# Kernel tuning notes

Measured on AMD Instinct MI355X. Metric: run time of the kernel, lower is better.

## Reference

```python
import jax, jax.numpy as jnp
import numpy as np

B = 8192      # batch of matchups
L = 40        # history_len
HN = 32       # hist_numeric_dim
TE = 96       # team_embed_dim
SE = 32       # seed_embed_dim
HH = 64       # hist_hidden_dim
NH = 4        # num_heads
HD = HH // NH # head dim = 16
MID = 128     # middle_dim
BOX = 8       # box_score_dim
NT = 400      # num_teams
NS = 17       # num_seeds
TOWER_IN = TE + SE + 1 + 2 * HH  # 257
MERGED = 2 * MID                 # 256
EPS = 1e-5


def setup_inputs() -> dict:
    key = jax.random.key(0)
    ks = iter(jax.random.split(key, 80))
    nrm = lambda shape, s=0.05: (jax.random.normal(next(ks), shape, jnp.float32) * s)
    inp = {}
    inp['teamA_id'] = jax.random.randint(next(ks), (B,), 1, NT)
    inp['teamB_id'] = jax.random.randint(next(ks), (B,), 1, NT)
    inp['teamA_seed'] = jax.random.randint(next(ks), (B,), 0, NS)
    inp['teamB_seed'] = jax.random.randint(next(ks), (B,), 0, NS)
    inp['teamA_elo'] = 1500.0 + 200.0 * jax.random.normal(next(ks), (B,), jnp.float32)
    inp['teamB_elo'] = 1500.0 + 200.0 * jax.random.normal(next(ks), (B,), jnp.float32)
    inp['teamA_hist_numeric'] = jax.random.normal(next(ks), (B, L, HN), jnp.float32)
    inp['teamB_hist_numeric'] = jax.random.normal(next(ks), (B, L, HN), jnp.float32)
    inp['teamA_hist_opp_ids'] = jax.random.randint(next(ks), (B, L), 0, NT)
    inp['teamB_hist_opp_ids'] = jax.random.randint(next(ks), (B, L), 0, NT)
    # 0/1 padding mask; guarantee at least one valid game per row
    inp['teamA_hist_mask'] = (jax.random.uniform(next(ks), (B, L)) < 0.8).astype(jnp.float32).at[:, 0].set(1.0)
    inp['teamB_hist_mask'] = (jax.random.uniform(next(ks), (B, L)) < 0.8).astype(jnp.float32).at[:, 0].set(1.0)
    # parameters
    inp['team_emb'] = nrm((NT, TE), 0.1).at[0].set(0.0)  # padding_idx=0
    inp['seed_emb'] = nrm((NS, SE), 0.1)
    inp['conv_w'] = nrm((HH, HN + TE, 3))
    inp['conv_b'] = nrm((HH,))
    inp['cbn_g'] = jnp.ones((HH,)); inp['cbn_b'] = jnp.zeros((HH,))
    inp['cbn_rm'] = nrm((HH,), 0.01); inp['cbn_rv'] = jnp.ones((HH,))
    inp['hp_w'] = nrm((HH, HN + TE)); inp['hp_b'] = nrm((HH,))
    inp['qp_w'] = nrm((HH, TE)); inp['qp_b'] = nrm((HH,))
    inp['attn_in_w'] = nrm((3 * HH, HH)); inp['attn_in_b'] = nrm((3 * HH,))
    inp['attn_out_w'] = nrm((HH, HH)); inp['attn_out_b'] = nrm((HH,))
    inp['ln_g'] = jnp.ones((HH,)); inp['ln_b'] = jnp.zeros((HH,))
    inp['tw_w'] = nrm((MID, TOWER_IN)); inp['tw_b'] = nrm((MID,))
    inp['tbn_g'] = jnp.ones((MID,)); inp['tbn_b'] = jnp.zeros((MID,))
    inp['tbn_rm'] = nrm((MID,), 0.01); inp['tbn_rv'] = jnp.ones((MID,))
    inp['r1_w'] = nrm((MERGED, MERGED)); inp['r1_b'] = nrm((MERGED,))
    inp['r1bn_g'] = jnp.ones((MERGED,)); inp['r1bn_b'] = jnp.zeros((MERGED,))
    inp['r1bn_rm'] = nrm((MERGED,), 0.01); inp['r1bn_rv'] = jnp.ones((MERGED,))
    inp['r2_w'] = nrm((MERGED, MERGED)); inp['r2_b'] = nrm((MERGED,))
    inp['r2bn_g'] = jnp.ones((MERGED,)); inp['r2bn_b'] = jnp.zeros((MERGED,))
    inp['r2bn_rm'] = nrm((MERGED,), 0.01); inp['r2bn_rv'] = jnp.ones((MERGED,))
    inp['mu_w'] = nrm((BOX, MERGED)); inp['mu_b'] = nrm((BOX,))
    inp['lv_w'] = nrm((BOX, MERGED)); inp['lv_b'] = nrm((BOX,))
    inp['wl_w'] = nrm((1, MERGED)); inp['wl_b'] = nrm((1,))
    return inp


def _bn(x, g, b, rm, rv):
    # eval-mode BatchNorm over last axis
    return (x - rm) * jax.lax.rsqrt(rv + EPS) * g + b


def _ln(x, g, b):
    m = jnp.mean(x, axis=-1, keepdims=True)
    v = jnp.var(x, axis=-1, keepdims=True)
    return (x - m) * jax.lax.rsqrt(v + EPS) * g + b


def reference(teamA_id, teamB_id, teamA_seed, teamB_seed, teamA_elo, teamB_elo,
              teamA_hist_numeric, teamA_hist_opp_ids, teamA_hist_mask,
              teamB_hist_numeric, teamB_hist_opp_ids, teamB_hist_mask,
              team_emb, seed_emb, conv_w, conv_b, cbn_g, cbn_b, cbn_rm, cbn_rv,
              hp_w, hp_b, qp_w, qp_b, attn_in_w, attn_in_b, attn_out_w, attn_out_b,
              ln_g, ln_b, tw_w, tw_b, tbn_g, tbn_b, tbn_rm, tbn_rv,
              r1_w, r1_b, r1bn_g, r1bn_b, r1bn_rm, r1bn_rv,
              r2_w, r2_b, r2bn_g, r2bn_b, r2bn_rm, r2bn_rv,
              mu_w, mu_b, lv_w, lv_b, wl_w, wl_b):
    silu = jax.nn.silu

    def attend(q_emb, hn, opp, mask):
        m = mask[..., None]
        x = jnp.concatenate([hn * m, team_emb[opp] * m], axis=-1)      # [B,L,HN+TE]
        res = silu(x @ hp_w.T + hp_b)                                   # [B,L,HH]
        c = jax.lax.conv_general_dilated(
            x.transpose(0, 2, 1), conv_w, (1,), [(1, 1)],
            dimension_numbers=('NCH', 'OIH', 'NCH')) + conv_b[:, None]  # [B,HH,L]
        c = _bn(c.transpose(0, 2, 1), cbn_g, cbn_b, cbn_rm, cbn_rv)     # [B,L,HH]
        kv = silu(c + res)                                              # [B,L,HH]
        q = q_emb @ qp_w.T + qp_b                                       # [B,HH]
        wq, wk, wv = jnp.split(attn_in_w, 3, axis=0)
        bq, bk, bv = jnp.split(attn_in_b, 3, axis=0)
        qh = (q @ wq.T + bq).reshape(-1, NH, HD)
        kh = (kv @ wk.T + bk).reshape(-1, L, NH, HD)
        vh = (kv @ wv.T + bv).reshape(-1, L, NH, HD)
        scores = jnp.einsum('bhd,blhd->bhl', qh, kh) / np.float32(np.sqrt(HD))
        scores = jnp.where(mask[:, None, :] > 0.0, scores, -1e9)
        a = jax.nn.softmax(scores, axis=-1)
        o = jnp.einsum('bhl,blhd->bhd', a, vh).reshape(-1, HH)
        o = o @ attn_out_w.T + attn_out_b
        return _ln(o + q, ln_g, ln_b)

    ea = team_emb[teamA_id]
    eb = team_emb[teamB_id]
    sa = seed_emb[teamA_seed]
    sb = seed_emb[teamB_seed]
    za = (teamA_elo[:, None] - 1500.0) / 400.0
    zb = (teamB_elo[:, None] - 1500.0) / 400.0

    aa = attend(ea, teamA_hist_numeric, teamA_hist_opp_ids, teamA_hist_mask)
    ab = attend(ea, teamB_hist_numeric, teamB_hist_opp_ids, teamB_hist_mask)
    bb = attend(eb, teamB_hist_numeric, teamB_hist_opp_ids, teamB_hist_mask)
    ba = attend(eb, teamA_hist_numeric, teamA_hist_opp_ids, teamA_hist_mask)

    ta = jnp.concatenate([ea, sa, za, aa, ab], axis=-1)
    tb = jnp.concatenate([eb, sb, zb, bb, ba], axis=-1)

    tower = lambda t: silu(_bn(t @ tw_w.T + tw_b, tbn_g, tbn_b, tbn_rm, tbn_rv))
    ra = tower(ta)
    rb = tower(tb)

    x = jnp.concatenate([ra - rb, ra * rb], axis=-1)
    x = silu(_bn(x @ r1_w.T + r1_b, r1bn_g, r1bn_b, r1bn_rm, r1bn_rv)) + x
    x = silu(_bn(x @ r2_w.T + r2_b, r2bn_g, r2bn_b, r2bn_rm, r2bn_rv)) + x

    box_mu = x @ mu_w.T + mu_b
    box_log_var = x @ lv_w.T + lv_b
    win_logit = (x @ wl_w.T + wl_b)[:, 0]
    return ((box_mu, box_log_var), win_logit)
```

## Files before the change

### kernel.cpp

```cpp
#include <hip/hip_runtime.h>
#include <stdint.h>

#define EPS 1e-5f

typedef __attribute__((ext_vector_type(8))) short short8;
typedef __attribute__((ext_vector_type(4))) float floatx4;
typedef __attribute__((ext_vector_type(4))) unsigned uintx4;
typedef unsigned short u16;

__device__ __forceinline__ u16 f2bf(float f) {
  unsigned u = __builtin_bit_cast(unsigned, f);
  u += 0x7fffu + ((u >> 16) & 1u);
  return (u16)(u >> 16);
}
__device__ __forceinline__ float bf2f(u16 h) {
  return __builtin_bit_cast(float, (unsigned)h << 16);
}
__device__ __forceinline__ unsigned pack2bf(float a, float b) {
  return (unsigned)f2bf(a) | ((unsigned)f2bf(b) << 16);
}
__device__ __forceinline__ float silu_f(float x) { return x / (1.f + __expf(-x)); }
__device__ __forceinline__ float wave_sum(float x) {
  for (int off = 32; off > 0; off >>= 1) x += __shfl_xor(x, off);
  return x;
}

__global__ void prep_kernel(const float* __restrict__ hp_w, const float* __restrict__ conv_w,
                            const float* __restrict__ attn_in_w,
                            const float* __restrict__ attn_out_w,
                            const float* __restrict__ tw_w, const float* __restrict__ r1_w,
                            const float* __restrict__ r2_w,
                            u16* __restrict__ w1f, u16* __restrict__ w2f,
                            float* __restrict__ woT,
                            float* __restrict__ twT, float* __restrict__ r1T,
                            float* __restrict__ r2T) {
  int t = blockIdx.x * 256 + threadIdx.x;
  if (t < 32768) {
    int j = t & 7, lane = (t >> 3) & 63, ks = (t >> 9) & 3, nt = (t >> 11) & 3, tp = t >> 13;
    int k = ks * 32 + ((lane >> 4) << 3) + j;
    int c = nt * 16 + (lane & 15);
    float v = (tp == 3) ? hp_w[c * 128 + k] : conv_w[c * 384 + k * 3 + tp];
    w1f[t] = f2bf(v);
  }
  if (t < 8192) {
    int j = t & 7, lane = (t >> 3) & 63, ks = (t >> 9) & 1, nt = t >> 10;
    int k = ks * 32 + ((lane >> 4) << 3) + j;
    int n = nt * 16 + (lane & 15);
    w2f[t] = f2bf(attn_in_w[(64 + n) * 64 + k]);
  }
  if (t < 1024) {
    int j = t & 63, k4 = t >> 6;
#pragma unroll
    for (int i = 0; i < 4; ++i)
      woT[(k4 * 64 + j) * 4 + i] = attn_out_w[j * 64 + k4 * 4 + i];
  }
  if (t < 8320) {
    int mid = t & 127, k4 = t >> 7;
#pragma unroll
    for (int i = 0; i < 4; ++i) {
      int k = k4 * 4 + i;
      twT[t * 4 + i] = (k < 257) ? tw_w[mid * 257 + k] : 0.f;
    }
  }
  if (t < 16384) {
    int o = t & 255, k4 = t >> 8;
#pragma unroll
    for (int i = 0; i < 4; ++i) {
      r1T[t * 4 + i] = r1_w[o * 256 + k4 * 4 + i];
      r2T[t * 4 + i] = r2_w[o * 256 + k4 * 4 + i];
    }
  }
}

__global__ __launch_bounds__(64) void team_kernel(
    const float* __restrict__ temb, const float* __restrict__ qp_w,
    const float* __restrict__ qp_b, const float* __restrict__ attn_in_w,
    const float* __restrict__ attn_in_b,
    float* __restrict__ Qg, float* __restrict__ QHg) {
  __shared__ float e[96];
  __shared__ float qv[64];
  const int t = blockIdx.x;
  const int o = threadIdx.x;
  for (int i = o; i < 96; i += 64) e[i] = temb[t * 96 + i];
  __syncthreads();
  float acc = qp_b[o];
  for (int k = 0; k < 96; ++k) acc += e[k] * qp_w[o * 96 + k];
  qv[o] = acc;
  Qg[t * 64 + o] = acc;
  __syncthreads();
  float acc2 = attn_in_b[o];
  for (int k = 0; k < 64; ++k) acc2 += qv[k] * attn_in_w[o * 64 + k];
  QHg[t * 64 + o] = acc2;
}

__global__ __launch_bounds__(256, 2) void attn_kernel(
    const int* __restrict__ idA, const int* __restrict__ idB,
    const float* __restrict__ hnA, const float* __restrict__ hnB,
    const int* __restrict__ oppA, const int* __restrict__ oppB,
    const float* __restrict__ mskA, const float* __restrict__ mskB,
    const float* __restrict__ temb, const float* __restrict__ conv_b,
    const float* __restrict__ cbn_g, const float* __restrict__ cbn_b,
    const float* __restrict__ cbn_rm, const float* __restrict__ cbn_rv,
    const float* __restrict__ hp_b,
    const float* __restrict__ attn_in_b, const float* __restrict__ attn_out_b,
    const float* __restrict__ ln_g, const float* __restrict__ ln_b,
    const u16* __restrict__ w1f, const u16* __restrict__ w2f,
    const float* __restrict__ woT,
    const float* __restrict__ Qg, const float* __restrict__ QHg,
    float* __restrict__ ATT) {
  __shared__ __align__(16) u16 arena[19488];
  __shared__ __align__(16) float qh_s[2 * 64];
  u16* xs = arena;
  u16* kvb = arena + 5712;
  float* KVP = (float*)(arena + 9168);
  float* a_s = (float*)(arena + 5712);
  float* op = a_s + 8 * 40;

  const int tid = threadIdx.x;
  const int lane = tid & 63;
  const int wv = tid >> 6;
  const int qd = lane >> 4;
  const int l16 = lane & 15;
  const int qw = wv >> 1;
  const int hw = wv & 1;

  const int c_lane = wv * 16 + l16;
  const float sc_c = rsqrtf(cbn_rv[c_lane] + EPS) * cbn_g[c_lane];
  const float sh_c = cbn_b[c_lane] - cbn_rm[c_lane] * sc_c;
  const float hpb_c = hp_b[c_lane];
  const float cvb_c = conv_b[c_lane];
  const float lng = ln_g[lane], lnb = ln_b[lane];
  const float aob = attn_out_b[lane];
  const float kb0 = attn_in_b[64 + (wv * 2 + 0) * 16 + l16];
  const float kb1 = attn_in_b[64 + (wv * 2 + 1) * 16 + l16];

  if (tid < 136) {
    xs[tid] = 0;
    xs[41 * 136 + tid] = 0;
  }
  __syncthreads();

  short8 w1r[4][4];
#pragma unroll
  for (int tp = 0; tp < 4; ++tp)
#pragma unroll
    for (int ks = 0; ks < 4; ++ks)
      w1r[tp][ks] = *reinterpret_cast<const short8*>(
          w1f + (((tp * 4 + wv) * 4 + ks) * 64 + lane) * 8);
  short8 w2r[2][2];
#pragma unroll
  for (int ntl = 0; ntl < 2; ++ntl)
#pragma unroll
    for (int ks = 0; ks < 2; ++ks)
      w2r[ntl][ks] = *reinterpret_cast<const short8*>(
          w2f + (((wv * 2 + ntl) * 2 + ks) * 64 + lane) * 8);

  unsigned xr[12];
  float mkr[3];
  {
    int np = blockIdx.x;
    int pb = np >> 1;
    const float* phn = (np & 1) ? hnB : hnA;
    const int* popp = (np & 1) ? oppB : oppA;
    const float* pmsk = (np & 1) ? mskB : mskA;
#pragma unroll
    for (int j = 0; j < 3; ++j) {
      int sidx = j * 256 + tid;
      int srow = sidx >> 4, scg = sidx & 15;
      if (srow < 40) {
        int mrow = pb * 40 + srow;
        mkr[j] = pmsk[mrow];
        const float* p = (scg < 4)
                             ? phn + (size_t)mrow * 32 + scg * 8
                             : temb + (size_t)popp[mrow] * 96 + (scg * 8 - 32);
        floatx4 f0 = *reinterpret_cast<const floatx4*>(p);
        floatx4 f1 = *reinterpret_cast<const floatx4*>(p + 4);
        xr[j * 4 + 0] = pack2bf(f0[0], f0[1]);
        xr[j * 4 + 1] = pack2bf(f0[2], f0[3]);
        xr[j * 4 + 2] = pack2bf(f1[0], f1[1]);
        xr[j * 4 + 3] = pack2bf(f1[2], f1[3]);
      } else {
        mkr[j] = 0.f;
        xr[j * 4 + 0] = xr[j * 4 + 1] = xr[j * 4 + 2] = xr[j * 4 + 3] = 0u;
      }
    }
  }

  float qreg = 0.f, qhreg = 0.f, m_l = 0.f;
  {
    int b0i = blockIdx.x >> 1, s0 = blockIdx.x & 1;
    if (lane < 40) m_l = (s0 ? mskB : mskA)[b0i * 40 + lane];
    if (wv < 2) {
      int id0 = wv ? idB[b0i] : idA[b0i];
      qreg = Qg[id0 * 64 + lane];
      qhreg = QHg[id0 * 64 + lane];
    }
  }

#pragma unroll 1
  for (int it = 0; it < 8; ++it) {
    int pair = blockIdx.x + it * 2048;
    int b = pair >> 1, s = pair & 1;

#pragma unroll
    for (int j = 0; j < 3; ++j) {
      int sidx = j * 256 + tid;
      int srow = sidx >> 4;
      if (srow < 40) {
        bool keep = mkr[j] != 0.f;
        uintx4 v;
        v[0] = keep ? xr[j * 4 + 0] : 0u;
        v[1] = keep ? xr[j * 4 + 1] : 0u;
        v[2] = keep ? xr[j * 4 + 2] : 0u;
        v[3] = keep ? xr[j * 4 + 3] : 0u;
        *reinterpret_cast<uintx4*>(xs + (srow + 1) * 136 + (sidx & 15) * 8) = v;
      }
    }
    __syncthreads();

    float pf[3][8];
    float mknew[3];
    {
      int np = (it < 7) ? pair + 2048 : pair;
      int pb = np >> 1;
      const float* phn = (np & 1) ? hnB : hnA;
      const int* popp = (np & 1) ? oppB : oppA;
      const float* pmsk = (np & 1) ? mskB : mskA;
#pragma unroll
      for (int j = 0; j < 3; ++j) {
        int sidx = j * 256 + tid;
        int srow = sidx >> 4, scg = sidx & 15;
        if (srow < 40) {
          int mrow = pb * 40 + srow;
          mknew[j] = pmsk[mrow];
          const float* p = (scg < 4)
                               ? phn + (size_t)mrow * 32 + scg * 8
                               : temb + (size_t)popp[mrow] * 96 + (scg * 8 - 32);
          *reinterpret_cast<floatx4*>(&pf[j][0]) = *reinterpret_cast<const floatx4*>(p);
          *reinterpret_cast<floatx4*>(&pf[j][4]) = *reinterpret_cast<const floatx4*>(p + 4);
        } else {
          mknew[j] = 0.f;
#pragma unroll
          for (int q = 0; q < 8; ++q) pf[j][q] = 0.f;
        }
      }
    }

#pragma unroll 1
    for (int mt = 0; mt < 3; ++mt) {
      floatx4 ach = {0.f, 0.f, 0.f, 0.f};
      floatx4 acv = {0.f, 0.f, 0.f, 0.f};
#pragma unroll
      for (int ks = 0; ks < 4; ++ks) {
        const u16* base = xs + (mt * 16 + l16) * 136 + ks * 32 + (qd << 3);
        short8 af0 = *reinterpret_cast<const short8*>(base);
        short8 af1 = *reinterpret_cast<const short8*>(base + 136);
        short8 af2 = *reinterpret_cast<const short8*>(base + 272);
        acv = __builtin_amdgcn_mfma_f32_16x16x32_bf16(af0, w1r[0][ks], acv, 0, 0, 0);
        acv = __builtin_amdgcn_mfma_f32_16x16x32_bf16(af1, w1r[1][ks], acv, 0, 0, 0);
        acv = __builtin_amdgcn_mfma_f32_16x16x32_bf16(af2, w1r[2][ks], acv, 0, 0, 0);
        ach = __builtin_amdgcn_mfma_f32_16x16x32_bf16(af1, w1r[3][ks], ach, 0, 0, 0);
      }
#pragma unroll
      for (int r = 0; r < 4; ++r) {
        float kv = silu_f(silu_f(ach[r] + hpb_c) + (acv[r] + cvb_c) * sc_c + sh_c);
        kvb[(mt * 16 + qd * 4 + r) * 72 + c_lane] = f2bf(kv);
      }
    }
    if (wv < 2) qh_s[wv * 64 + lane] = qhreg;
    __syncthreads();

    {
      floatx4 acc[3][2] = {};
#pragma unroll
      for (int mt = 0; mt < 3; ++mt) {
        short8 af[2];
#pragma unroll
        for (int ks = 0; ks < 2; ++ks)
          af[ks] = *reinterpret_cast<const short8*>(
              kvb + (mt * 16 + l16) * 72 + ks * 32 + (qd << 3));
#pragma unroll
        for (int ntl = 0; ntl < 2; ++ntl)
#pragma unroll
          for (int ks = 0; ks < 2; ++ks)
            acc[mt][ntl] = __builtin_amdgcn_mfma_f32_16x16x32_bf16(
                af[ks], w2r[ntl][ks], acc[mt][ntl], 0, 0, 0);
      }
#pragma unroll
      for (int mt = 0; mt < 3; ++mt)
#pragma unroll
        for (int ntl = 0; ntl < 2; ++ntl)
#pragma unroll
          for (int r = 0; r < 4; ++r) {
            int row = mt * 16 + qd * 4 + r;
            if (row < 40)
              KVP[row * 129 + (wv * 2 + ntl) * 16 + l16] =
                  acc[mt][ntl][r] + (ntl ? kb1 : kb0);
          }
    }
    __syncthreads();

#pragma unroll
    for (int j = 0; j < 3; ++j) {
      xr[j * 4 + 0] = pack2bf(pf[j][0], pf[j][1]);
      xr[j * 4 + 1] = pack2bf(pf[j][2], pf[j][3]);
      xr[j * 4 + 2] = pack2bf(pf[j][4], pf[j][5]);
      xr[j * 4 + 3] = pack2bf(pf[j][6], pf[j][7]);
      mkr[j] = mknew[j];
    }

    {
      float a2[2];
#pragma unroll
      for (int hh = 0; hh < 2; ++hh) {
        int h = hw * 2 + hh;
        float e = 0.f;
        if (lane < 40 && m_l > 0.f) {
          float s0 = 0.f, s1 = 0.f;
#pragma unroll
          for (int d = 0; d < 16; d += 2) {
            s0 += qh_s[qw * 64 + h * 16 + d] * KVP[lane * 129 + h * 16 + d];
            s1 += qh_s[qw * 64 + h * 16 + d + 1] * KVP[lane * 129 + h * 16 + d + 1];
          }
          e = __expf((s0 + s1) * 0.25f);
        }
        float sm = wave_sum(e);
        a2[hh] = e / sm;
      }
      if (lane < 40) {
        a_s[(qw * 4 + hw * 2 + 0) * 40 + lane] = a2[0];
        a_s[(qw * 4 + hw * 2 + 1) * 40 + lane] = a2[1];
      }
    }

    {
      int d = hw * 32 + (lane & 31);
      int arow = qw * 4 + (d >> 4);
      int l0 = (lane >> 5) * 20;
      float v0 = 0.f, v1 = 0.f;
#pragma unroll
      for (int li = 0; li < 20; li += 2) {
        int l = l0 + li;
        v0 += a_s[arow * 40 + l] * KVP[l * 129 + 64 + d];
        v1 += a_s[arow * 40 + l + 1] * KVP[(l + 1) * 129 + 64 + d];
      }
      float v = v0 + v1;
      v += __shfl_xor(v, 32);
      if (lane < 32) op[qw * 64 + d] = v;
    }
    __syncthreads();

    if (wv < 2) {
      int qi = wv;
      float acc0 = aob + qreg, acc1 = 0.f;
      const floatx4* wo4 = reinterpret_cast<const floatx4*>(woT);
#pragma unroll 8
      for (int k4 = 0; k4 < 16; ++k4) {
        floatx4 w4 = wo4[k4 * 64 + lane];
        floatx4 x4 = *reinterpret_cast<const floatx4*>(&op[qi * 64 + k4 * 4]);
        acc0 += x4[0] * w4[0] + x4[2] * w4[2];
        acc1 += x4[1] * w4[1] + x4[3] * w4[3];
      }
      float r = acc0 + acc1;
      float mean = wave_sum(r) * (1.f / 64.f);
      float dv = r - mean;
      float var = wave_sum(dv * dv) * (1.f / 64.f);
      float outv = dv * rsqrtf(var + EPS) * lng + lnb;
      ATT[((qi * 2 + s) * 8192 + b) * 64 + lane] = outv;
    }

    if (it < 7) {
      int bn = b + 1024;
      if (lane < 40) m_l = (s ? mskB : mskA)[bn * 40 + lane];
      if (wv < 2) {
        int idn = wv ? idB[bn] : idA[bn];
        qreg = Qg[idn * 64 + lane];
        qhreg = QHg[idn * 64 + lane];
      }
    }
  }
}

__global__ __launch_bounds__(256) void head_kernel(
    const int* __restrict__ idA, const int* __restrict__ idB,
    const int* __restrict__ seedA, const int* __restrict__ seedB,
    const float* __restrict__ eloA, const float* __restrict__ eloB,
    const float* __restrict__ temb, const float* __restrict__ semb,
    const float* __restrict__ twT, const float* __restrict__ tw_b,
    const float* __restrict__ tbn_g, const float* __restrict__ tbn_b,
    const float* __restrict__ tbn_rm, const float* __restrict__ tbn_rv,
    const float* __restrict__ r1T, const float* __restrict__ r1_b,
    const float* __restrict__ r1bn_g, const float* __restrict__ r1bn_b,
    const float* __restrict__ r1bn_rm, const float* __restrict__ r1bn_rv,
    const float* __restrict__ r2T, const float* __restrict__ r2_b,
    const float* __restrict__ r2bn_g, const float* __restrict__ r2bn_b,
    const float* __restrict__ r2bn_rm, const float* __restrict__ r2bn_rv,
    const float* __restrict__ mu_w, const float* __restrict__ mu_b,
    const float* __restrict__ lv_w, const float* __restrict__ lv_b,
    const float* __restrict__ wl_w, const float* __restrict__ wl_b,
    const float* __restrict__ ATT, float* __restrict__ out) {
  __shared__ __align__(16) float smem[12416];
  float* tv = smem;
  float* rr = smem + 8320;
  float* xv = smem;
  float* xw = smem + 4096;
  const int tid = threadIdx.x;
  const int b0 = blockIdx.x * 16;

  for (int idx = tid; idx < 2 * 16 * 260; idx += 256) {
    int k = idx % 260;
    int bi = (idx / 260) & 15;
    int team = idx / (260 * 16);
    int b = b0 + bi;
    float v;
    if (k < 96) v = temb[(team ? idB[b] : idA[b]) * 96 + k];
    else if (k < 128) v = semb[(team ? seedB[b] : seedA[b]) * 32 + (k - 96)];
    else if (k == 128) v = ((team ? eloB[b] : eloA[b]) - 1500.f) * (1.f / 400.f);
    else if (k < 193) v = ATT[((team * 2 + team) * 8192 + b) * 64 + (k - 129)];
    else if (k < 257) v = ATT[((team * 2 + (1 - team)) * 8192 + b) * 64 + (k - 193)];
    else v = 0.f;
    tv[(team * 16 + bi) * 260 + k] = v;
  }
  __syncthreads();

  {
    int team = tid >> 7, mid = tid & 127;
    const floatx4* twv = reinterpret_cast<const floatx4*>(twT);
    float acc[16];
    float b_ = tw_b[mid];
#pragma unroll
    for (int bi = 0; bi < 16; ++bi) acc[bi] = b_;
#pragma unroll 2
    for (int k4 = 0; k4 < 65; ++k4) {
      floatx4 w4 = twv[k4 * 128 + mid];
#pragma unroll
      for (int bi = 0; bi < 16; ++bi) {
        floatx4 x4 = *reinterpret_cast<const floatx4*>(&tv[(team * 16 + bi) * 260 + k4 * 4]);
        acc[bi] += x4[0] * w4[0] + x4[1] * w4[1] + x4[2] * w4[2] + x4[3] * w4[3];
      }
    }
    float sc = rsqrtf(tbn_rv[mid] + EPS) * tbn_g[mid];
    float sh = tbn_b[mid] - tbn_rm[mid] * sc;
#pragma unroll
    for (int bi = 0; bi < 16; ++bi)
      rr[(team * 16 + bi) * 128 + mid] = silu_f(acc[bi] * sc + sh);
  }
  __syncthreads();
  {
    int o = tid;
#pragma unroll
    for (int bi = 0; bi < 16; ++bi)
      xv[bi * 256 + o] = (o < 128)
                             ? (rr[bi * 128 + o] - rr[(16 + bi) * 128 + o])
                             : (rr[bi * 128 + o - 128] * rr[(16 + bi) * 128 + o - 128]);
  }
  __syncthreads();
  {
    int o = tid;
    const floatx4* r1v = reinterpret_cast<const floatx4*>(r1T);
    float acc[16];
    float b_ = r1_b[o];
#pragma unroll
    for (int bi = 0; bi < 16; ++bi) acc[bi] = b_;
#pragma unroll 2
    for (int k4 = 0; k4 < 64; ++k4) {
      floatx4 w4 = r1v[k4 * 256 + o];
#pragma unroll
      for (int bi = 0; bi < 16; ++bi) {
        floatx4 x4 = *reinterpret_cast<const floatx4*>(&xv[bi * 256 + k4 * 4]);
        acc[bi] += x4[0] * w4[0] + x4[1] * w4[1] + x4[2] * w4[2] + x4[3] * w4[3];
      }
    }
    float sc = rsqrtf(r1bn_rv[o] + EPS) * r1bn_g[o];
    float sh = r1bn_b[o] - r1bn_rm[o] * sc;
#pragma unroll
    for (int bi = 0; bi < 16; ++bi)
      xw[bi * 256 + o] = silu_f(acc[bi] * sc + sh) + xv[bi * 256 + o];
  }
  __syncthreads();
  {
    int o = tid;
    const floatx4* r2v = reinterpret_cast<const floatx4*>(r2T);
    float acc[16];
    float b_ = r2_b[o];
#pragma unroll
    for (int bi = 0; bi < 16; ++bi) acc[bi] = b_;
#pragma unroll 2
    for (int k4 = 0; k4 < 64; ++k4) {
      floatx4 w4 = r2v[k4 * 256 + o];
#pragma unroll
      for (int bi = 0; bi < 16; ++bi) {
        floatx4 x4 = *reinterpret_cast<const floatx4*>(&xw[bi * 256 + k4 * 4]);
        acc[bi] += x4[0] * w4[0] + x4[1] * w4[1] + x4[2] * w4[2] + x4[3] * w4[3];
      }
    }
    float sc = rsqrtf(r2bn_rv[o] + EPS) * r2bn_g[o];
    float sh = r2bn_b[o] - r2bn_rm[o] * sc;
#pragma unroll
    for (int bi = 0; bi < 16; ++bi)
      xv[bi * 256 + o] = silu_f(acc[bi] * sc + sh) + xw[bi * 256 + o];
  }
  __syncthreads();
  {
    int bi = tid >> 4, j = tid & 15;
    const float* wrow = (j < 8) ? (mu_w + j * 256) : (lv_w + (j - 8) * 256);
    const floatx4* wrow4 = reinterpret_cast<const floatx4*>(wrow);
    float acc = (j < 8) ? mu_b[j] : lv_b[j - 8];
#pragma unroll 4
    for (int k4 = 0; k4 < 64; ++k4) {
      floatx4 x4 = *reinterpret_cast<const floatx4*>(&xv[bi * 256 + k4 * 4]);
      floatx4 w4 = wrow4[k4];
      acc += x4[0] * w4[0] + x4[1] * w4[1] + x4[2] * w4[2] + x4[3] * w4[3];
    }
    int b = b0 + bi;
    if (j < 8) out[b * 8 + j] = acc;
    else out[65536 + b * 8 + (j - 8)] = acc;
    if (tid < 16) {
      const floatx4* wl4 = reinterpret_cast<const floatx4*>(wl_w);
      float acc2 = wl_b[0];
#pragma unroll 4
      for (int k4 = 0; k4 < 64; ++k4) {
        floatx4 x4 = *reinterpret_cast<const floatx4*>(&xv[tid * 256 + k4 * 4]);
        floatx4 w4 = wl4[k4];
        acc2 += x4[0] * w4[0] + x4[1] * w4[1] + x4[2] * w4[2] + x4[3] * w4[3];
      }
      out[131072 + b0 + tid] = acc2;
    }
  }
}

extern "C" void kernel_launch(void* const* d_in, const int* in_sizes, int n_in,
                              void* d_out, int out_size, void* d_ws, size_t ws_size,
                              hipStream_t stream) {
  const int* idA = (const int*)d_in[0];
  const int* idB = (const int*)d_in[1];
  const int* seedA = (const int*)d_in[2];
  const int* seedB = (const int*)d_in[3];
  const float* eloA = (const float*)d_in[4];
  const float* eloB = (const float*)d_in[5];
  const float* hnA = (const float*)d_in[6];
  const float* hnB = (const float*)d_in[7];
  const int* oppA = (const int*)d_in[8];
  const int* oppB = (const int*)d_in[9];
  const float* mskA = (const float*)d_in[10];
  const float* mskB = (const float*)d_in[11];
  const float* temb = (const float*)d_in[12];
  const float* semb = (const float*)d_in[13];
  const float* conv_w = (const float*)d_in[14];
  const float* conv_b = (const float*)d_in[15];
  const float* cbn_g = (const float*)d_in[16];
  const float* cbn_b = (const float*)d_in[17];
  const float* cbn_rm = (const float*)d_in[18];
  const float* cbn_rv = (const float*)d_in[19];
  const float* hp_w = (const float*)d_in[20];
  const float* hp_b = (const float*)d_in[21];
  const float* qp_w = (const float*)d_in[22];
  const float* qp_b = (const float*)d_in[23];
  const float* attn_in_w = (const float*)d_in[24];
  const float* attn_in_b = (const float*)d_in[25];
  const float* attn_out_w = (const float*)d_in[26];
  const float* attn_out_b = (const float*)d_in[27];
  const float* ln_g = (const float*)d_in[28];
  const float* ln_b = (const float*)d_in[29];
  const float* tw_w = (const float*)d_in[30];
  const float* tw_b = (const float*)d_in[31];
  const float* tbn_g = (const float*)d_in[32];
  const float* tbn_b = (const float*)d_in[33];
  const float* tbn_rm = (const float*)d_in[34];
  const float* tbn_rv = (const float*)d_in[35];
  const float* r1_w = (const float*)d_in[36];
  const float* r1_b = (const float*)d_in[37];
  const float* r1bn_g = (const float*)d_in[38];
  const float* r1bn_b = (const float*)d_in[39];
  const float* r1bn_rm = (const float*)d_in[40];
  const float* r1bn_rv = (const float*)d_in[41];
  const float* r2_w = (const float*)d_in[42];
  const float* r2_b = (const float*)d_in[43];
  const float* r2bn_g = (const float*)d_in[44];
  const float* r2bn_b = (const float*)d_in[45];
  const float* r2bn_rm = (const float*)d_in[46];
  const float* r2bn_rv = (const float*)d_in[47];
  const float* mu_w = (const float*)d_in[48];
  const float* mu_b = (const float*)d_in[49];
  const float* lv_w = (const float*)d_in[50];
  const float* lv_b = (const float*)d_in[51];
  const float* wl_w = (const float*)d_in[52];
  const float* wl_b = (const float*)d_in[53];

  char* ws = (char*)d_ws;
  u16* w1f = (u16*)(ws + 0);
  u16* w2f = (u16*)(ws + 65536);
  float* woT = (float*)(ws + 81920);
  float* Qg = (float*)(ws + 98304);
  float* QHg = (float*)(ws + 200704);
  float* twT = (float*)(ws + 303104);
  float* r1T = (float*)(ws + 436224);
  float* r2T = (float*)(ws + 698368);
  float* ATT = (float*)(ws + 960512);

  prep_kernel<<<256, 256, 0, stream>>>(hp_w, conv_w, attn_in_w, attn_out_w,
                                       tw_w, r1_w, r2_w,
                                       w1f, w2f, woT, twT, r1T, r2T);
  team_kernel<<<400, 64, 0, stream>>>(temb, qp_w, qp_b, attn_in_w, attn_in_b, Qg, QHg);
  attn_kernel<<<2048, 256, 0, stream>>>(idA, idB, hnA, hnB, oppA, oppB, mskA, mskB,
                                        temb, conv_b, cbn_g, cbn_b, cbn_rm, cbn_rv,
                                        hp_b, attn_in_b, attn_out_b, ln_g, ln_b,
                                        w1f, w2f, woT, Qg, QHg, ATT);
  head_kernel<<<512, 256, 0, stream>>>(idA, idB, seedA, seedB, eloA, eloB, temb, semb,
                                       twT, tw_b, tbn_g, tbn_b, tbn_rm, tbn_rv,
                                       r1T, r1_b, r1bn_g, r1bn_b, r1bn_rm, r1bn_rv,
                                       r2T, r2_b, r2bn_g, r2bn_b, r2bn_rm, r2bn_rv,
                                       mu_w, mu_b, lv_w, lv_b, wl_w, wl_b,
                                       ATT, (float*)d_out);
}
```

Measured before the change: 535.7 us.

## Prefetch opponent ids and query vectors one extra iteration ahead in attend loop

The opponent-id indices used for the embedding gather are now loaded two iterations ahead, so the next iteration's team-embedding loads no longer wait on a dependent index load. The per-pair query, head-query and mask loads move from the loop tail into the prefetch block, overlapping them with the MFMA work. The bf16 packing of prefetched rows moves earlier, and the initial barrier is merged with the first prefetch. This adds register pressure from extra live values.

```diff
diff --git a/kernel.cpp b/kernel.cpp
--- a/kernel.cpp
+++ b/kernel.cpp
@@ -138,7 +138,6 @@
     xs[tid] = 0;
     xs[41 * 136 + tid] = 0;
   }
-  __syncthreads();
 
   short8 w1r[4][4];
 #pragma unroll
@@ -187,6 +186,8 @@
   }
 
   float qreg = 0.f, qhreg = 0.f, m_l = 0.f;
+  int idn = 0;
+  int oppn[3];
   {
     int b0i = blockIdx.x >> 1, s0 = blockIdx.x & 1;
     if (lane < 40) m_l = (s0 ? mskB : mskA)[b0i * 40 + lane];
@@ -194,8 +195,18 @@
       int id0 = wv ? idB[b0i] : idA[b0i];
       qreg = Qg[id0 * 64 + lane];
       qhreg = QHg[id0 * 64 + lane];
-    }
-  }
+      idn = wv ? idB[b0i + 1024] : idA[b0i + 1024];
+    }
+    int np1 = blockIdx.x + 2048;
+    int pb1 = np1 >> 1;
+    const int* popp1 = (np1 & 1) ? oppB : oppA;
+#pragma unroll
+    for (int j = 0; j < 3; ++j) {
+      int srow = (j * 256 + tid) >> 4;
+      oppn[j] = (srow < 40) ? popp1[pb1 * 40 + srow] : 0;
+    }
+  }
+  __syncthreads();
 
 #pragma unroll 1
   for (int it = 0; it < 8; ++it) {
@@ -220,11 +231,12 @@
 
     float pf[3][8];
     float mknew[3];
+    float m_n = 0.f, qn = 0.f, qhn = 0.f;
+    int idn2 = 0;
     {
       int np = (it < 7) ? pair + 2048 : pair;
       int pb = np >> 1;
       const float* phn = (np & 1) ? hnB : hnA;
-      const int* popp = (np & 1) ? oppB : oppA;
       const float* pmsk = (np & 1) ? mskB : mskA;
 #pragma unroll
       for (int j = 0; j < 3; ++j) {
@@ -235,7 +247,7 @@
           mknew[j] = pmsk[mrow];
           const float* p = (scg < 4)
                                ? phn + (size_t)mrow * 32 + scg * 8
-                               : temb + (size_t)popp[mrow] * 96 + (scg * 8 - 32);
+                               : temb + (size_t)oppn[j] * 96 + (scg * 8 - 32);
           *reinterpret_cast<floatx4*>(&pf[j][0]) = *reinterpret_cast<const floatx4*>(p);
           *reinterpret_cast<floatx4*>(&pf[j][4]) = *reinterpret_cast<const floatx4*>(p + 4);
         } else {
@@ -244,6 +256,20 @@
           for (int q = 0; q < 8; ++q) pf[j][q] = 0.f;
         }
       }
+      if (lane < 40) m_n = pmsk[pb * 40 + lane];
+      if (wv < 2) {
+        qn = Qg[idn * 64 + lane];
+        qhn = QHg[idn * 64 + lane];
+      }
+      int np2 = (it < 6) ? pair + 4096 : pair;
+      int pb2 = np2 >> 1;
+      const int* popp2 = (np2 & 1) ? oppB : oppA;
+#pragma unroll
+      for (int j = 0; j < 3; ++j) {
+        int srow = (j * 256 + tid) >> 4;
+        oppn[j] = (srow < 40) ? popp2[pb2 * 40 + srow] : 0;
+      }
+      if (wv < 2) idn2 = wv ? idB[pb2] : idA[pb2];
     }
 
 #pragma unroll 1
@@ -270,6 +296,15 @@
     if (wv < 2) qh_s[wv * 64 + lane] = qhreg;
     __syncthreads();
 
+#pragma unroll
+    for (int j = 0; j < 3; ++j) {
+      xr[j * 4 + 0] = pack2bf(pf[j][0], pf[j][1]);
+      xr[j * 4 + 1] = pack2bf(pf[j][2], pf[j][3]);
+      xr[j * 4 + 2] = pack2bf(pf[j][4], pf[j][5]);
+      xr[j * 4 + 3] = pack2bf(pf[j][6], pf[j][7]);
+      mkr[j] = mknew[j];
+    }
+
     {
       floatx4 acc[3][2] = {};
 #pragma unroll
@@ -299,15 +334,6 @@
           }
     }
     __syncthreads();
-
-#pragma unroll
-    for (int j = 0; j < 3; ++j) {
-      xr[j * 4 + 0] = pack2bf(pf[j][0], pf[j][1]);
-      xr[j * 4 + 1] = pack2bf(pf[j][2], pf[j][3]);
-      xr[j * 4 + 2] = pack2bf(pf[j][4], pf[j][5]);
-      xr[j * 4 + 3] = pack2bf(pf[j][6], pf[j][7]);
-      mkr[j] = mknew[j];
-    }
 
     {
       float a2[2];
@@ -369,15 +395,10 @@
       ATT[((qi * 2 + s) * 8192 + b) * 64 + lane] = outv;
     }
 
-    if (it < 7) {
-      int bn = b + 1024;
-      if (lane < 40) m_l = (s ? mskB : mskA)[bn * 40 + lane];
-      if (wv < 2) {
-        int idn = wv ? idB[bn] : idA[bn];
-        qreg = Qg[idn * 64 + lane];
-        qhreg = QHg[idn * 64 + lane];
-      }
-    }
+    qreg = qn;
+    qhreg = qhn;
+    m_l = m_n;
+    idn = idn2;
   }
 }
 
```

New measurement: 529.9 us. No clear change (-1.1%).
